# Performance work log

Measured on AMD Instinct MI355X. Metric: run time of the kernel, lower is better.

The kernel has to match this reference:

```python
import jax, jax.numpy as jnp
import numpy as np

NUM_STEPS = 3
NUM_POINTS = 5
LENGTH = 1.0
MAXVAL = float(np.sinh(LENGTH))


def setup_inputs() -> dict:
    key = jax.random.key(0)
    k1, k2, k3 = jax.random.split(key, 3)
    data = jax.random.normal(k1, (64, 128, 64, 64), jnp.float32)
    # control tables: row 0 = values at knots, row 1 = tangents (Hermite)
    velocity = jnp.concatenate(
        [jnp.linspace(0.0, 1.0, NUM_POINTS)[None, :],
         jnp.full((1, NUM_POINTS), 2.0 * np.pi / NUM_POINTS)], axis=0).astype(jnp.float32)
    angles = jnp.concatenate(
        [jnp.linspace(0.0, 2.0 * np.pi, NUM_POINTS)[None, :],
         jnp.full((1, NUM_POINTS), 2.0 * np.pi / NUM_POINTS)], axis=0).astype(jnp.float32)
    channel_transform = jax.random.normal(k2, (1, 1), jnp.float32)
    spatio_transform = jax.random.normal(k3, (1, 1), jnp.float32)
    return {"data": data, "velocity": velocity, "angles": angles,
            "channel_transform": channel_transform, "spatio_transform": spatio_transform}


def _handler(x):
    # bucketize x into one of the NUM_POINTS-1 spline segments (unit-width knots)
    t = jnp.clip(x, 0.0, float(NUM_POINTS - 1))
    i0 = jnp.clip(jnp.floor(t).astype(jnp.int32), 0, NUM_POINTS - 2)
    u = t - i0.astype(x.dtype)
    return i0, u


def _hermite(table, i0, u):
    v, m = table[0], table[1]  # values, tangents at knots
    u2 = u * u
    u3 = u2 * u
    h00 = 2.0 * u3 - 3.0 * u2 + 1.0
    h10 = u3 - 2.0 * u2 + u
    h01 = -2.0 * u3 + 3.0 * u2
    h11 = u3 - u2
    return h00 * v[i0] + h10 * m[i0] + h01 * v[i0 + 1] + h11 * m[i0 + 1]


def reference(data, velocity, angles, channel_transform, spatio_transform):
    B, C, H, W = data.shape
    x = data * MAXVAL
    x = x.reshape(B, C, H * W).transpose(0, 2, 1)  # (B, HW, C)
    x = x * channel_transform[0, 0]                # (.., 1) @ (1, 1) == scalar mul
    step = LENGTH / NUM_STEPS
    for _ in range(NUM_STEPS):
        i0, u = _handler(x)
        vel = _hermite(velocity, i0, u)
        ang = _hermite(angles, i0, u)
        x = x + (vel * jnp.cos(ang) + x * vel * jnp.sin(ang)) * step
    x = x * spatio_transform[0, 0]
    x = x.transpose(0, 2, 1).reshape(B, C, H, W)
    return x / MAXVAL
```

## Files before the change

kernel.cpp:

```cpp
#include <hip/hip_runtime.h>


#define MAXVAL_F 1.1752011936438014f

typedef float nfloat4 __attribute__((ext_vector_type(4)));

constexpr int   TAB_N  = 1024;
constexpr float TAB_L0 = -0.5f;
constexpr float TAB_H  = 5.0f / (float)TAB_N;
constexpr int   ITER   = 8;
constexpr int   BLK    = 256;
constexpr int   F4_PER_BLOCK = BLK * ITER;

__device__ __forceinline__ float eval_exact(float x,
    const float* __restrict__ vt, const float* __restrict__ at) {
#pragma unroll
  for (int k = 0; k < 3; ++k) {
    float t = fminf(fmaxf(x, 0.0f), 4.0f);
    int i0 = (int)t;
    if (i0 > 3) i0 = 3;
    float u  = t - (float)i0;
    float u2 = u * u, u3 = u2 * u;
    float h00 =  2.0f * u3 - 3.0f * u2 + 1.0f;
    float h10 =         u3 - 2.0f * u2 + u;
    float h01 = -2.0f * u3 + 3.0f * u2;
    float h11 =         u3 -        u2;
    float vel = h00 * vt[i0] + h10 * vt[5 + i0] + h01 * vt[i0 + 1] + h11 * vt[6 + i0];
    float ang = h00 * at[i0] + h10 * at[5 + i0] + h01 * at[i0 + 1] + h11 * at[6 + i0];
    float sn = sinf(ang);
    float cs = cosf(ang);
    x = x + (vel * cs + x * vel * sn) * (1.0f / 3.0f);
  }
  return x;
}

__global__ void build_table_kernel(const float* __restrict__ vt,
                                   const float* __restrict__ at,
                                   const float* __restrict__ stp,
                                   float2* __restrict__ gtab) {
  int j = blockIdx.x * blockDim.x + threadIdx.x;
  if (j >= TAB_N) return;
  float sc = stp[0] * (1.0f / MAXVAL_F);
  float x0 = TAB_L0 + TAB_H * (float)j;
  float x1 = TAB_L0 + TAB_H * (float)(j + 1);
  float g0 = eval_exact(x0, vt, at) * sc;
  float g1 = eval_exact(x1, vt, at) * sc;
  gtab[j] = make_float2(g0, g1 - g0);
}

__device__ __forceinline__ float lerp_tab(float x, float C1, float C0,
                                          const float2* __restrict__ tab) {
  float s  = fmaf(x, C1, C0);
  float fj = floorf(s);
  fj = fminf(fmaxf(fj, 0.0f), (float)(TAB_N - 2));
  float u  = s - fj;
  float2 e = tab[(int)fj];
  return fmaf(u, e.y, e.x);
}

__device__ __forceinline__ void nt_store4(float4 o, float4* p) {
  nfloat4 v = {o.x, o.y, o.z, o.w};
  __builtin_nontemporal_store(v, (nfloat4*)p);
}

__global__ __launch_bounds__(BLK) void apply_map_kernel(
    const float4* __restrict__ in, float4* __restrict__ out,
    const float2* __restrict__ gtab, const float* __restrict__ ctp, int nf4) {
  __shared__ float2 tab[TAB_N];
  {
    const float4* g4 = (const float4*)gtab;
    float4* t4 = (float4*)tab;
#pragma unroll
    for (int i = 0; i < 2; ++i)
      t4[(int)threadIdx.x + i * BLK] = g4[(int)threadIdx.x + i * BLK];
  }
  float C1 = ctp[0] * (MAXVAL_F / TAB_H);
  const float C0 = -TAB_L0 / TAB_H;
  __syncthreads();

  int base = (int)blockIdx.x * F4_PER_BLOCK + (int)threadIdx.x;

  if (base + (ITER - 1) * BLK < nf4) {
    float4 d[ITER];
#pragma unroll
    for (int k = 0; k < ITER; ++k) d[k] = in[base + k * BLK];
#pragma unroll
    for (int k = 0; k < ITER; ++k) {
      float4 o;
      o.x = lerp_tab(d[k].x, C1, C0, tab);
      o.y = lerp_tab(d[k].y, C1, C0, tab);
      o.z = lerp_tab(d[k].z, C1, C0, tab);
      o.w = lerp_tab(d[k].w, C1, C0, tab);
      nt_store4(o, &out[base + k * BLK]);
    }
  } else {
#pragma unroll
    for (int k = 0; k < ITER; ++k) {
      int idx = base + k * BLK;
      if (idx < nf4) {
        float4 d = in[idx];
        float4 o;
        o.x = lerp_tab(d.x, C1, C0, tab);
        o.y = lerp_tab(d.y, C1, C0, tab);
        o.z = lerp_tab(d.z, C1, C0, tab);
        o.w = lerp_tab(d.w, C1, C0, tab);
        nt_store4(o, &out[idx]);
      }
    }
  }
}

extern "C" void kernel_launch(void* const* d_in, const int* in_sizes, int n_in,
                              void* d_out, int out_size, void* d_ws, size_t ws_size,
                              hipStream_t stream) {
  const float* data = (const float*)d_in[0];
  const float* vel  = (const float*)d_in[1];
  const float* ang  = (const float*)d_in[2];
  const float* ct   = (const float*)d_in[3];
  const float* st   = (const float*)d_in[4];
  float*       outp = (float*)d_out;
  float2*      gtab = (float2*)d_ws;

  hipLaunchKernelGGL(build_table_kernel, dim3((TAB_N + 255) / 256), dim3(256), 0, stream,
                     vel, ang, st, gtab);

  int n   = in_sizes[0];
  int nf4 = n / 4;
  int blocks = (nf4 + F4_PER_BLOCK - 1) / F4_PER_BLOCK;
  hipLaunchKernelGGL(apply_map_kernel, dim3(blocks), dim3(BLK), 0, stream,
                     (const float4*)data, (float4*)outp, gtab, ct, nf4);
}
```

Baseline: 241.9 us.

## Replicate lookup table across LDS banks to avoid bank conflicts

Shrinks the precomputed map table to 512 scalar knots and stores 16 interleaved copies in shared memory, with each lane reading the copy chosen by its thread index so that random gathers land in separate LDS banks. Each lookup becomes two scalar reads and an interpolation, replacing one float2 read. The cost is a larger 32 KB shared-memory fill per block, a coarser table with possibly more interpolation error, and an added occupancy hint in the launch bounds.

```diff
diff --git a/kernel.cpp b/kernel.cpp
--- a/kernel.cpp
+++ b/kernel.cpp
@@ -5,9 +5,11 @@
 
 typedef float nfloat4 __attribute__((ext_vector_type(4)));
 
-constexpr int   TAB_N  = 1024;
+constexpr int   TAB_K  = 512;
+constexpr int   REP    = 16;
 constexpr float TAB_L0 = -0.5f;
-constexpr float TAB_H  = 5.0f / (float)TAB_N;
+constexpr float TAB_HI = 4.5f;
+constexpr float INV_H  = (float)(TAB_K - 1) / (TAB_HI - TAB_L0);
 constexpr int   ITER   = 8;
 constexpr int   BLK    = 256;
 constexpr int   F4_PER_BLOCK = BLK * ITER;
@@ -37,25 +39,12 @@
 __global__ void build_table_kernel(const float* __restrict__ vt,
                                    const float* __restrict__ at,
                                    const float* __restrict__ stp,
-                                   float2* __restrict__ gtab) {
+                                   float* __restrict__ gtab) {
   int j = blockIdx.x * blockDim.x + threadIdx.x;
-  if (j >= TAB_N) return;
+  if (j >= TAB_K) return;
   float sc = stp[0] * (1.0f / MAXVAL_F);
-  float x0 = TAB_L0 + TAB_H * (float)j;
-  float x1 = TAB_L0 + TAB_H * (float)(j + 1);
-  float g0 = eval_exact(x0, vt, at) * sc;
-  float g1 = eval_exact(x1, vt, at) * sc;
-  gtab[j] = make_float2(g0, g1 - g0);
-}
-
-__device__ __forceinline__ float lerp_tab(float x, float C1, float C0,
-                                          const float2* __restrict__ tab) {
-  float s  = fmaf(x, C1, C0);
-  float fj = floorf(s);
-  fj = fminf(fmaxf(fj, 0.0f), (float)(TAB_N - 2));
-  float u  = s - fj;
-  float2 e = tab[(int)fj];
-  return fmaf(u, e.y, e.x);
+  float x  = TAB_L0 + (float)j / INV_H;
+  gtab[j] = eval_exact(x, vt, at) * sc;
 }
 
 __device__ __forceinline__ void nt_store4(float4 o, float4* p) {
@@ -63,19 +52,31 @@
   __builtin_nontemporal_store(v, (nfloat4*)p);
 }
 
-__global__ __launch_bounds__(BLK) void apply_map_kernel(
+__device__ __forceinline__ float lerp_tab(float x, float C1, float C0, int lrep,
+                                          const float* __restrict__ vrep) {
+  float s  = fmaf(x, C1, C0);
+  float fj = fminf(fmaxf(floorf(s), 0.0f), (float)(TAB_K - 2));
+  float u  = s - fj;
+  int   off = ((int)fj << 4) | lrep;
+  float a0 = vrep[off];
+  float a1 = vrep[off + REP];
+  return fmaf(u, a1 - a0, a0);
+}
+
+__global__ __launch_bounds__(BLK, 4) void apply_map_kernel(
     const float4* __restrict__ in, float4* __restrict__ out,
-    const float2* __restrict__ gtab, const float* __restrict__ ctp, int nf4) {
-  __shared__ float2 tab[TAB_N];
+    const float* __restrict__ gtab, const float* __restrict__ ctp, int nf4) {
+  __shared__ float vrep[TAB_K * REP];
   {
-    const float4* g4 = (const float4*)gtab;
-    float4* t4 = (float4*)tab;
 #pragma unroll
-    for (int i = 0; i < 2; ++i)
-      t4[(int)threadIdx.x + i * BLK] = g4[(int)threadIdx.x + i * BLK];
+    for (int k = 0; k < (TAB_K * REP) / BLK; ++k) {
+      int i = (int)threadIdx.x + k * BLK;
+      vrep[i] = gtab[i >> 4];
+    }
   }
-  float C1 = ctp[0] * (MAXVAL_F / TAB_H);
-  const float C0 = -TAB_L0 / TAB_H;
+  float C1 = ctp[0] * (MAXVAL_F * INV_H);
+  const float C0 = -TAB_L0 * INV_H;
+  int lrep = (int)threadIdx.x & (REP - 1);
   __syncthreads();
 
   int base = (int)blockIdx.x * F4_PER_BLOCK + (int)threadIdx.x;
@@ -87,10 +88,10 @@
 #pragma unroll
     for (int k = 0; k < ITER; ++k) {
       float4 o;
-      o.x = lerp_tab(d[k].x, C1, C0, tab);
-      o.y = lerp_tab(d[k].y, C1, C0, tab);
-      o.z = lerp_tab(d[k].z, C1, C0, tab);
-      o.w = lerp_tab(d[k].w, C1, C0, tab);
+      o.x = lerp_tab(d[k].x, C1, C0, lrep, vrep);
+      o.y = lerp_tab(d[k].y, C1, C0, lrep, vrep);
+      o.z = lerp_tab(d[k].z, C1, C0, lrep, vrep);
+      o.w = lerp_tab(d[k].w, C1, C0, lrep, vrep);
       nt_store4(o, &out[base + k * BLK]);
     }
   } else {
@@ -100,10 +101,10 @@
       if (idx < nf4) {
         float4 d = in[idx];
         float4 o;
-        o.x = lerp_tab(d.x, C1, C0, tab);
-        o.y = lerp_tab(d.y, C1, C0, tab);
-        o.z = lerp_tab(d.z, C1, C0, tab);
-        o.w = lerp_tab(d.w, C1, C0, tab);
+        o.x = lerp_tab(d.x, C1, C0, lrep, vrep);
+        o.y = lerp_tab(d.y, C1, C0, lrep, vrep);
+        o.z = lerp_tab(d.z, C1, C0, lrep, vrep);
+        o.w = lerp_tab(d.w, C1, C0, lrep, vrep);
         nt_store4(o, &out[idx]);
       }
     }
@@ -119,9 +120,9 @@
   const float* ct   = (const float*)d_in[3];
   const float* st   = (const float*)d_in[4];
   float*       outp = (float*)d_out;
-  float2*      gtab = (float2*)d_ws;
+  float*       gtab = (float*)d_ws;
 
-  hipLaunchKernelGGL(build_table_kernel, dim3((TAB_N + 255) / 256), dim3(256), 0, stream,
+  hipLaunchKernelGGL(build_table_kernel, dim3((TAB_K + 255) / 256), dim3(256), 0, stream,
                      vel, ang, st, gtab);
 
   int n   = in_sizes[0];
```

New measurement: 241.0 us. No clear change (-0.4%).
